# Performance work log

Measured on AMD Instinct MI355X. Metric: run time of the kernel, lower is better.

Reference implementation:

```python
import jax, jax.numpy as jnp
import numpy as np

B, S, HID, NH, HD = 2, 2048, 1024, 16, 64  # batch, seq, hidden, heads, head_dim (1024//NH)
ROPE_THETA = 10000.0
EPS = 1e-5


def _ternary_quantize(w):
    # BitNet b1.58 absmean weight quantization: ternary values + scalar scale.
    s = jnp.mean(jnp.abs(w)) + EPS
    q = jnp.clip(jnp.round(w / s), -1.0, 1.0)
    return q, s


def _rotate_half(x):
    x1, x2 = jnp.split(x, 2, axis=-1)
    return jnp.concatenate((-x2, x1), axis=-1)


def _rope_cos_sin(position_ids, head_dim, dtype):
    inv_freq = 1.0 / (ROPE_THETA ** (jnp.arange(0, head_dim, 2, dtype=jnp.float32) / head_dim))
    freqs = position_ids.astype(jnp.float32)[..., None] * inv_freq  # [b, s, hd/2]
    emb = jnp.concatenate((freqs, freqs), axis=-1)  # [b, s, hd]
    # add head axis -> [b, 1, s, hd]
    return jnp.cos(emb)[:, None].astype(dtype), jnp.sin(emb)[:, None].astype(dtype)


def setup_inputs() -> dict:
    key = jax.random.key(0)
    ks = jax.random.split(key, 5)
    hidden_states = jax.random.normal(ks[0], (B, S, HID), jnp.float32)
    hidden_states_scale = jnp.ones((1,), jnp.float32)
    position_ids = jnp.broadcast_to(jnp.arange(S, dtype=jnp.int32), (B, S))
    wq = jax.random.normal(ks[1], (HID, HID), jnp.float32) * 0.02
    wk = jax.random.normal(ks[2], (HID, HID), jnp.float32) * 0.02
    wv = jax.random.normal(ks[3], (HID, HID), jnp.float32) * 0.02
    wo = jax.random.normal(ks[4], (HID, HID), jnp.float32) * 0.02
    return {"hidden_states": hidden_states, "hidden_states_scale": hidden_states_scale,
            "position_ids": position_ids, "wq": wq, "wk": wk, "wv": wv, "wo": wo}


def reference(hidden_states, hidden_states_scale, position_ids, wq, wk, wv, wo):
    b, s, _ = hidden_states.shape
    hs_scale = hidden_states_scale.reshape(())

    # QuantizedLinear: ternary weight values, scale carried separately.
    wq_q, sq = _ternary_quantize(wq)
    wk_q, sk = _ternary_quantize(wk)
    wv_q, sv = _ternary_quantize(wv)
    wo_q, so = _ternary_quantize(wo)

    # Projections in the quantized-value domain: out = x @ Wq^T, out_scale = x_scale * w_scale
    q = jnp.einsum('bsh,oh->bso', hidden_states, wq_q)
    k = jnp.einsum('bsh,oh->bso', hidden_states, wk_q)
    v = jnp.einsum('bsh,oh->bso', hidden_states, wv_q)
    q_scale = hs_scale * sq
    k_scale = hs_scale * sk
    v_scale = hs_scale * sv

    # [b, nh, s, hd]
    q = q.reshape(b, s, NH, HD).transpose(0, 2, 1, 3)
    k = k.reshape(b, s, NH, HD).transpose(0, 2, 1, 3)
    v = v.reshape(b, s, NH, HD).transpose(0, 2, 1, 3)

    cos, sin = _rope_cos_sin(position_ids, HD, q.dtype)
    q = q * cos + _rotate_half(q) * sin
    k = k * cos + _rotate_half(k) * sin

    # quantized_matmul(Q, qs, K, ks): values multiply, scales multiply (scale unused by softmax,
    # matching the original which softmaxes the quantized-domain scores).
    attn = jnp.einsum('bhqd,bhkd->bhqk', q, k).astype(jnp.float32) * (1.0 / np.sqrt(HD))
    attn = jax.nn.softmax(attn, axis=-1)

    # quantized_matmul(attn, 1.0, V, vs)
    out = jnp.einsum('bhqk,bhkd->bhqd', attn, v.astype(jnp.float32))
    out_scale = 1.0 * v_scale

    out = out.transpose(0, 2, 1, 3).reshape(b, s, HID)
    out = jnp.einsum('bsh,oh->bso', out, wo_q)
    out_scale = out_scale * so
    return out, out_scale
```

## Files before the change

kernel.cpp:

```cpp
#include <hip/hip_runtime.h>
#include <hip/hip_bf16.h>

#define NB 2
#define NS 2048
#define NHID 1024
#define NHEAD 16
#define NHD 64
#define NTOK (NB*NS)
#define WELEM (NHID*NHID)

typedef unsigned short u16;
typedef __attribute__((ext_vector_type(4))) float floatx4;
typedef __attribute__((ext_vector_type(16))) float floatx16;
typedef __attribute__((ext_vector_type(8))) __bf16 bf16x8;
typedef __attribute__((ext_vector_type(8))) unsigned short ushort8;
typedef __attribute__((ext_vector_type(4))) unsigned short ushort4v;
typedef __attribute__((ext_vector_type(2))) unsigned uint2v;

__device__ __forceinline__ u16 f2bf(float f) {
  union { float f; unsigned u; } a; a.f = f;
  unsigned u = a.u;
  unsigned r = (u + 0x7fffu + ((u >> 16) & 1u)) >> 16;
  return (u16)r;
}
__device__ __forceinline__ float bf2f(u16 s) {
  union { unsigned u; float f; } a; a.u = ((unsigned)s) << 16;
  return a.f;
}
__device__ __forceinline__ void gload16(const void* g, void* lds) {
  __builtin_amdgcn_global_load_lds(
      (const __attribute__((address_space(1))) unsigned int*)g,
      (__attribute__((address_space(3))) unsigned int*)lds, 16, 0, 0);
}
__device__ __forceinline__ uint2v pl32(unsigned a, unsigned b) {
  return __builtin_amdgcn_permlane32_swap(a, b, false, false);
}
__device__ __forceinline__ float mergemax(float x) {
  uint2v r = pl32(__float_as_uint(x), __float_as_uint(x));
  return fmaxf(__uint_as_float(r[0]), __uint_as_float(r[1]));
}
__device__ __forceinline__ float mergesum(float x) {
  uint2v r = pl32(__float_as_uint(x), __float_as_uint(x));
  return __uint_as_float(r[0]) + __uint_as_float(r[1]);
}
__device__ __forceinline__ float tmax16(const floatx16& v) {
  float a = fmaxf(fmaxf(fmaxf(v[0], v[1]), fmaxf(v[2], v[3])),
                  fmaxf(fmaxf(v[4], v[5]), fmaxf(v[6], v[7])));
  float b = fmaxf(fmaxf(fmaxf(v[8], v[9]), fmaxf(v[10], v[11])),
                  fmaxf(fmaxf(v[12], v[13]), fmaxf(v[14], v[15])));
  return fmaxf(a, b);
}

__global__ void k_init(double* sums) { if (threadIdx.x < 4) sums[threadIdx.x] = 0.0; }

__global__ void k_abssum(const float* __restrict__ wq, const float* __restrict__ wk,
                         const float* __restrict__ wv, const float* __restrict__ wo,
                         double* __restrict__ sums) {
  const float* srcs[4] = {wq, wk, wv, wo};
  const float* w = srcs[blockIdx.y];
  int idx = (blockIdx.x * 256 + threadIdx.x) * 16;
  float s = 0.f;
#pragma unroll
  for (int j = 0; j < 4; j++) {
    float4 v = *(const float4*)(w + idx + j * 4);
    s += fabsf(v.x) + fabsf(v.y) + fabsf(v.z) + fabsf(v.w);
  }
#pragma unroll
  for (int off = 32; off; off >>= 1) s += __shfl_down(s, off);
  __shared__ float ps[4];
  if ((threadIdx.x & 63) == 0) ps[threadIdx.x >> 6] = s;
  __syncthreads();
  if (threadIdx.x == 0) atomicAdd(&sums[blockIdx.y], (double)(ps[0] + ps[1] + ps[2] + ps[3]));
}

__global__ void k_quantsplit(const float* __restrict__ wq, const float* __restrict__ wk,
                             const float* __restrict__ wv, const float* __restrict__ wo,
                             const double* __restrict__ sums, u16* __restrict__ wt,
                             const float* __restrict__ x,
                             u16* __restrict__ xh, u16* __restrict__ xl,
                             float2* __restrict__ rtab) {
  int bid = blockIdx.x;
  if (bid < 4096) {
    const float* srcs[4] = {wq, wk, wv, wo};
    int y = bid >> 10, xb = bid & 1023;
    const float* w = srcs[y];
    u16* dst = wt + y * WELEM;
    float s = (float)(sums[y] / (double)WELEM) + 1e-5f;
    int idx = (xb * 256 + threadIdx.x) * 4;
    float4 v = *(const float4*)(w + idx);
    float f[4] = {v.x, v.y, v.z, v.w};
    union { u16 ss[4]; uint2 u; } O;
#pragma unroll
    for (int j = 0; j < 4; j++) {
      float q = rintf(f[j] / s);
      q = fminf(1.f, fmaxf(-1.f, q));
      O.ss[j] = f2bf(q);
    }
    *(uint2*)(dst + idx) = O.u;
  } else if (bid < 8192) {
    int idx = ((bid - 4096) * 256 + threadIdx.x) * 4;
    float4 v = *(const float4*)(x + idx);
    float f[4] = {v.x, v.y, v.z, v.w};
    union { u16 s[4]; uint2 u; } H, L;
#pragma unroll
    for (int j = 0; j < 4; j++) {
      u16 hb = f2bf(f[j]);
      H.s[j] = hb;
      L.s[j] = f2bf(f[j] - bf2f(hb));
    }
    *(uint2*)(xh + idx) = H.u;
    *(uint2*)(xl + idx) = L.u;
  } else {
    int idx = (bid - 8192) * 256 + threadIdx.x;
    int d = idx & 31;
    float p = (float)(idx >> 5);
    float inv = exp2f((float)d * -0.4152410118609203f);
    float fr = p * inv;
    rtab[idx] = make_float2(cosf(fr), sinf(fr));
  }
}

template <int MODE>
__global__ __launch_bounds__(256) void k_gemm(
    const u16* __restrict__ Ahi, const u16* __restrict__ Alo,
    const u16* __restrict__ Wt, const int* __restrict__ pos_ids,
    const float2* __restrict__ rtab, float* __restrict__ outf,
    u16* __restrict__ qh, u16* __restrict__ ql,
    u16* __restrict__ kh, u16* __restrict__ kl,
    u16* __restrict__ vt) {
  constexpr int BUF = (MODE == 0) ? 24576 : 16384;
  __shared__ __attribute__((aligned(16))) char GSM[2 * BUF];
  const int tid = threadIdx.x;
  const int wave = tid >> 6, lane = tid & 63;
  const int lr = lane & 15, lh = lane >> 4;
  const int bm = blockIdx.x, bn = blockIdx.y, z = blockIdx.z;
  const u16* W = Wt + (MODE == 0 ? z : 3) * WELEM;
  const int wr = wave >> 1, wc = wave & 1;

  floatx4 acc[4][4];
#pragma unroll
  for (int i = 0; i < 4; i++)
#pragma unroll
    for (int j = 0; j < 4; j++) acc[i][j] = (floatx4){0.f, 0.f, 0.f, 0.f};

  const int e0 = tid * 8;
  const int row0 = e0 >> 5, col0 = e0 & 31;

  auto stage = [&](int k0, int nb) {
#pragma unroll
    for (int it = 0; it < 2; ++it) {
      int row = row0 + it * 64;
      gload16(Ahi + (bm * 128 + row) * 1024 + k0 + col0, GSM + nb + it * 4096 + wave * 1024);
      if (MODE == 0)
        gload16(Alo + (bm * 128 + row) * 1024 + k0 + col0, GSM + nb + 8192 + it * 4096 + wave * 1024);
      gload16(W + (bn * 128 + row) * 1024 + k0 + col0,
              GSM + nb + (MODE == 0 ? 16384 : 8192) + it * 4096 + wave * 1024);
    }
  };

  stage(0, 0);

  for (int kt = 0; kt < 32; ++kt) {
    __syncthreads();
    const int cb = (kt & 1) * BUF;
    if (kt < 31) stage((kt + 1) * 32, ((kt + 1) & 1) * BUF);

    const u16* Ahp = (const u16*)(GSM + cb);
    const u16* Bp  = (const u16*)(GSM + cb + (MODE == 0 ? 16384 : 8192));
    bf16x8 ah[4], bfr[4];
#pragma unroll
    for (int mi = 0; mi < 4; mi++)
      ah[mi] = *(const bf16x8*)(Ahp + (wr * 64 + mi * 16 + lr) * 32 + lh * 8);
#pragma unroll
    for (int ni = 0; ni < 4; ni++)
      bfr[ni] = *(const bf16x8*)(Bp + (wc * 64 + ni * 16 + lr) * 32 + lh * 8);
#pragma unroll
    for (int mi = 0; mi < 4; mi++)
#pragma unroll
      for (int ni = 0; ni < 4; ni++)
        acc[mi][ni] = __builtin_amdgcn_mfma_f32_16x16x32_bf16(ah[mi], bfr[ni], acc[mi][ni], 0, 0, 0);
    if (MODE == 0) {
      const u16* Alp = (const u16*)(GSM + cb + 8192);
      bf16x8 al8[4];
#pragma unroll
      for (int mi = 0; mi < 4; mi++)
        al8[mi] = *(const bf16x8*)(Alp + (wr * 64 + mi * 16 + lr) * 32 + lh * 8);
#pragma unroll
      for (int mi = 0; mi < 4; mi++)
#pragma unroll
        for (int ni = 0; ni < 4; ni++)
          acc[mi][ni] = __builtin_amdgcn_mfma_f32_16x16x32_bf16(al8[mi], bfr[ni], acc[mi][ni], 0, 0, 0);
    }
  }

  if (MODE == 1) {
#pragma unroll
    for (int mi = 0; mi < 4; mi++)
#pragma unroll
      for (int ni = 0; ni < 4; ni++)
#pragma unroll
        for (int i = 0; i < 4; i++) {
          int row = bm * 128 + wr * 64 + mi * 16 + lh * 4 + i;
          int col = bn * 128 + wc * 64 + ni * 16 + lr;
          outf[row * 1024 + col] = acc[mi][ni][i];
        }
    return;
  }

  const int hh = bn * 2 + wc;
  if (z == 2) {
#pragma unroll
    for (int mi = 0; mi < 4; mi++) {
      int row0v = bm * 128 + wr * 64 + mi * 16 + lh * 4;
      int bb = row0v >> 11, s_ = row0v & 2047;
      size_t vbase = ((size_t)(bb * NHEAD + hh)) * (NHD * NS) + s_;
#pragma unroll
      for (int ni = 0; ni < 4; ni++) {
        int hd = ni * 16 + lr;
        union { u16 s4[4]; ushort4v v; } V4;
#pragma unroll
        for (int i = 0; i < 4; i++) V4.s4[i] = f2bf(acc[mi][ni][i]);
        *(ushort4v*)(vt + vbase + (size_t)hd * NS) = V4.v;
      }
    }
    return;
  }

  const float qsc = (z == 0) ? 0.125f * 1.4426950408889634f : 1.0f;
  u16* dh = z ? kh : qh;
  u16* dl = z ? kl : ql;
  int posr[4][4];
#pragma unroll
  for (int mi = 0; mi < 4; mi++)
#pragma unroll
    for (int i = 0; i < 4; i++) {
      int row = bm * 128 + wr * 64 + mi * 16 + lh * 4 + i;
      posr[mi][i] = pos_ids[(row >> 11) * NS + (row & 2047)];
    }
#pragma unroll
  for (int ni = 0; ni < 2; ni++) {
    int d = ni * 16 + lr;
#pragma unroll
    for (int mi = 0; mi < 4; mi++)
#pragma unroll
      for (int i = 0; i < 4; i++) {
        int row = bm * 128 + wr * 64 + mi * 16 + lh * 4 + i;
        int bb = row >> 11, s_ = row & 2047;
        float2 cs = rtab[posr[mi][i] * 32 + d];
        float x1 = acc[mi][ni][i], x2 = acc[mi][ni + 2][i];
        float n1 = (x1 * cs.x - x2 * cs.y) * qsc;
        float n2 = (x2 * cs.x + x1 * cs.y) * qsc;
        size_t ob = ((size_t)(bb * NHEAD + hh) * NS + s_) * NHD + d;
        u16 h1 = f2bf(n1);
        dh[ob] = h1;      dl[ob] = f2bf(n1 - bf2f(h1));
        u16 h2 = f2bf(n2);
        dh[ob + 32] = h2; dl[ob + 32] = f2bf(n2 - bf2f(h2));
      }
  }
}

__global__ __launch_bounds__(512) void k_attn(
    const u16* __restrict__ qh, const u16* __restrict__ ql,
    const u16* __restrict__ kh, const u16* __restrict__ kl,
    const u16* __restrict__ vt, u16* __restrict__ aoh) {
  __shared__ __attribute__((aligned(16))) char SM[49152];
  const int tid = threadIdx.x, wave = tid >> 6, lane = tid & 63;
  const int l5 = lane & 31, hi = lane >> 5;
  const int bid = blockIdx.x;
  const int swzb = ((bid & 7) << 5) | (bid >> 3);
  const int qt = swzb & 7, bh = swzb >> 3;
  const int b = bh >> 4, hco = (bh & 15) * NHD;
  const int base = bh * (NS * NHD);
  const int qrow = qt * 256 + wave * 32 + l5;

  bf16x8 qfh[4], qfl[4];
#pragma unroll
  for (int s = 0; s < 4; s++) {
    int off = base + qrow * NHD + s * 16 + hi * 8;
    qfh[s] = *(const bf16x8*)(qh + off);
    qfl[s] = *(const bf16x8*)(ql + off);
  }

  const floatx16 Z16 = {};
  floatx16 acco[2];
  acco[0] = Z16; acco[1] = Z16;
  float m_r = -1e30f, l_r = 0.f;

  const char* khg0 = (const char*)(kh + base);
  const char* klg0 = (const char*)(kl + base);
  const char* vtg0 = (const char*)(vt + base);

#define STAGE_KV(key0_, nb_)                                                     \
  {                                                                              \
    const char* khg = khg0 + (key0_) * 128;                                      \
    const char* klg = klg0 + (key0_) * 128;                                      \
    const char* vtg = vtg0 + (key0_) * 2;                                        \
    int L = tid * 16;                                                            \
    int r7 = (L >> 7) & 7;                                                       \
    int g = L ^ (r7 << 4);                                                       \
    gload16(khg + g, SM + (nb_) + wave * 1024);                                  \
    gload16(klg + g, SM + (nb_) + 8192 + wave * 1024);                           \
    int vcol = (L & 127) ^ (r7 << 4);                                            \
    gload16(vtg + (size_t)(L >> 7) * 4096 + vcol,                                \
            SM + (nb_) + 16384 + wave * 1024);                                   \
  }

  STAGE_KV(0, 0);

  for (int kt = 0; kt < 32; ++kt) {
    __syncthreads();
    const int cb = (kt & 1) * 24576;
    const int key0 = kt * 64;

    if (kt < 31) STAGE_KV(key0 + 64, ((kt + 1) & 1) * 24576);

    floatx16 sacc[2];
#pragma unroll
    for (int t = 0; t < 2; t++) {
      const int row = 32 * t + l5;
      const int swz = (row & 7) << 4;
      {
        int byt = cb + row * 128 + ((hi * 16) ^ swz);
        bf16x8 ah = *(const bf16x8*)(SM + byt);
        bf16x8 al8 = *(const bf16x8*)(SM + 8192 + byt);
        __builtin_amdgcn_s_setprio(1);
        sacc[t] = __builtin_amdgcn_mfma_f32_32x32x16_bf16(ah, qfh[0], Z16, 0, 0, 0);
        sacc[t] = __builtin_amdgcn_mfma_f32_32x32x16_bf16(ah, qfl[0], sacc[t], 0, 0, 0);
        sacc[t] = __builtin_amdgcn_mfma_f32_32x32x16_bf16(al8, qfh[0], sacc[t], 0, 0, 0);
        __builtin_amdgcn_s_setprio(0);
      }
#pragma unroll
      for (int s = 1; s < 4; s++) {
        int byt = cb + row * 128 + ((s * 32 + hi * 16) ^ swz);
        bf16x8 ah = *(const bf16x8*)(SM + byt);
        bf16x8 al8 = *(const bf16x8*)(SM + 8192 + byt);
        __builtin_amdgcn_s_setprio(1);
        sacc[t] = __builtin_amdgcn_mfma_f32_32x32x16_bf16(ah, qfh[s], sacc[t], 0, 0, 0);
        sacc[t] = __builtin_amdgcn_mfma_f32_32x32x16_bf16(ah, qfl[s], sacc[t], 0, 0, 0);
        sacc[t] = __builtin_amdgcn_mfma_f32_32x32x16_bf16(al8, qfh[s], sacc[t], 0, 0, 0);
        __builtin_amdgcn_s_setprio(0);
      }
    }

    float mt = fmaxf(tmax16(sacc[0]), tmax16(sacc[1]));
    mt = mergemax(mt);
    if (!__all(mt <= m_r + 8.0f)) {
      float mn = fmaxf(m_r, mt);
      float sc2 = exp2f(m_r - mn);
      l_r *= sc2;
#pragma unroll
      for (int dt = 0; dt < 2; dt++)
#pragma unroll
        for (int r = 0; r < 16; r++) acco[dt][r] *= sc2;
      m_r = mn;
    }
    float s0 = 0.f, s1 = 0.f, s2 = 0.f, s3 = 0.f;
#pragma unroll
    for (int t = 0; t < 2; t++)
#pragma unroll
      for (int r = 0; r < 16; r += 4) {
        float p0 = exp2f(sacc[t][r + 0] - m_r);
        float p1 = exp2f(sacc[t][r + 1] - m_r);
        float p2 = exp2f(sacc[t][r + 2] - m_r);
        float p3 = exp2f(sacc[t][r + 3] - m_r);
        sacc[t][r + 0] = p0; sacc[t][r + 1] = p1;
        sacc[t][r + 2] = p2; sacc[t][r + 3] = p3;
        s0 += p0; s1 += p1; s2 += p2; s3 += p3;
      }
    l_r += mergesum((s0 + s1) + (s2 + s3));

    bf16x8 vtf[2][4];
#pragma unroll
    for (int dt = 0; dt < 2; dt++) {
      const int vrow = l5 + 32 * dt;
      const int swzv = (vrow & 7) << 4;
#pragma unroll
      for (int s = 0; s < 4; s++)
        vtf[dt][s] = *(const bf16x8*)(SM + cb + 16384 + vrow * 128 + ((s * 32 + hi * 16) ^ swzv));
    }

#pragma unroll
    for (int s = 0; s < 4; s++) {
      int t = s >> 1, rb = (s & 1) * 8;
      union { __bf16 bb[8]; unsigned u[4]; } Wp;
#pragma unroll
      for (int j = 0; j < 8; j++) Wp.bb[j] = (__bf16)sacc[t][rb + j];
      uint2v r02 = pl32(Wp.u[0], Wp.u[2]);
      uint2v r13 = pl32(Wp.u[1], Wp.u[3]);
      union { unsigned u[4]; bf16x8 v; } P;
      P.u[0] = r02[0]; P.u[1] = r13[0]; P.u[2] = r02[1]; P.u[3] = r13[1];
      __builtin_amdgcn_s_setprio(1);
      acco[0] = __builtin_amdgcn_mfma_f32_32x32x16_bf16(vtf[0][s], P.v, acco[0], 0, 0, 0);
      acco[1] = __builtin_amdgcn_mfma_f32_32x32x16_bf16(vtf[1][s], P.v, acco[1], 0, 0, 0);
      __builtin_amdgcn_s_setprio(0);
    }
  }

  float inv = 1.0f / l_r;
  float* OT = (float*)SM;
#pragma unroll
  for (int rnd = 0; rnd < 2; rnd++) {
    __syncthreads();
    if ((wave >> 2) == rnd) {
      int orow = (wave & 3) * 32 + l5;
#pragma unroll
      for (int dt = 0; dt < 2; dt++)
#pragma unroll
        for (int r = 0; r < 16; r++) {
          int col = (r & 3) + 8 * (r >> 2) + 4 * hi + 32 * dt;
          int cs = (col & 32) | ((col ^ l5) & 31);
          OT[orow * 64 + cs] = acco[dt][r] * inv;
        }
    }
    __syncthreads();
    {
      int row = tid >> 2, q4 = tid & 3;
      union { u16 s8[8]; ushort8 v; } HB[2];
#pragma unroll
      for (int j = 0; j < 16; j++) {
        int c = q4 * 16 + j;
        int cs = (c & 32) | ((c ^ (row & 31)) & 31);
        HB[j >> 3].s8[j & 7] = f2bf(OT[row * 64 + cs]);
      }
      int rowg = qt * 256 + rnd * 128 + row;
      size_t doff = ((size_t)(b * NS + rowg)) * NHID + hco + q4 * 16;
      *(ushort8*)(aoh + doff) = HB[0].v;
      *(ushort8*)(aoh + doff + 8) = HB[1].v;
    }
  }
}

__global__ void k_scale(const double* __restrict__ sums, const float* __restrict__ hss,
                        float* __restrict__ out) {
  if (threadIdx.x == 0) {
    float sv = (float)(sums[2] / (double)WELEM) + 1e-5f;
    float so = (float)(sums[3] / (double)WELEM) + 1e-5f;
    out[NTOK * NHID] = hss[0] * sv * so;
  }
}

extern "C" void kernel_launch(void* const* d_in, const int* in_sizes, int n_in,
                              void* d_out, int out_size, void* d_ws, size_t ws_size,
                              hipStream_t stream) {
  const float* x   = (const float*)d_in[0];
  const float* hss = (const float*)d_in[1];
  const int*   pos = (const int*)d_in[2];
  const float* wq  = (const float*)d_in[3];
  const float* wk  = (const float*)d_in[4];
  const float* wv  = (const float*)d_in[5];
  const float* wo  = (const float*)d_in[6];
  float* out = (float*)d_out;
  char* ws = (char*)d_ws;
  const size_t MB = 1u << 20;
  u16* wt = (u16*)(ws);
  u16* xh = (u16*)(ws + 8 * MB);
  u16* xl = (u16*)(ws + 16 * MB);
  u16* qh = (u16*)(ws + 24 * MB);
  u16* ql = (u16*)(ws + 32 * MB);
  u16* kh = (u16*)(ws + 40 * MB);
  u16* kl = (u16*)(ws + 48 * MB);
  u16* vt = (u16*)(ws + 56 * MB);
  double* sums = (double*)(ws + 72 * MB);
  float2* rtab = (float2*)(ws + 73 * MB);
  u16* aoh = xh;

  k_init<<<1, 64, 0, stream>>>(sums);
  k_abssum<<<dim3(256, 4), 256, 0, stream>>>(wq, wk, wv, wo, sums);
  k_quantsplit<<<8448, 256, 0, stream>>>(wq, wk, wv, wo, sums, wt, x, xh, xl, rtab);
  k_gemm<0><<<dim3(32, 8, 3), 256, 0, stream>>>(xh, xl, wt, pos, rtab, nullptr,
                                                qh, ql, kh, kl, vt);
  k_attn<<<256, 512, 0, stream>>>(qh, ql, kh, kl, vt, aoh);
  k_gemm<1><<<dim3(32, 8, 1), 256, 0, stream>>>(aoh, nullptr, wt, nullptr, nullptr, out,
                                                nullptr, nullptr, nullptr, nullptr, nullptr);
  k_scale<<<1, 64, 0, stream>>>(sums, hss, out);
}
```

Measured before the change: 204.1 us.

## Widen attention key tiles to 128, drop V low-part GEMM, fold scale kernel

The attention kernel now stages 128 keys per iteration instead of 64, doubling shared memory to 96KB and halving loop iterations and barriers. V fragments are read from LDS inside the PV loop rather than preloaded. The V projection skips its low-precision split MFMA pass, which halves its MMA work at some cost in accuracy. The init kernel becomes a memset and the scale kernel is folded into the output GEMM, removing launches. The larger LDS footprint may limit occupancy.

```diff
diff --git a/kernel.cpp b/kernel.cpp
--- a/kernel.cpp
+++ b/kernel.cpp
@@ -50,8 +50,6 @@
                   fmaxf(fmaxf(v[12], v[13]), fmaxf(v[14], v[15])));
   return fmaxf(a, b);
 }
-
-__global__ void k_init(double* sums) { if (threadIdx.x < 4) sums[threadIdx.x] = 0.0; }
 
 __global__ void k_abssum(const float* __restrict__ wq, const float* __restrict__ wk,
                          const float* __restrict__ wv, const float* __restrict__ wo,
@@ -127,7 +125,8 @@
     const float2* __restrict__ rtab, float* __restrict__ outf,
     u16* __restrict__ qh, u16* __restrict__ ql,
     u16* __restrict__ kh, u16* __restrict__ kl,
-    u16* __restrict__ vt) {
+    u16* __restrict__ vt,
+    const double* __restrict__ sums, const float* __restrict__ hss) {
   constexpr int BUF = (MODE == 0) ? 24576 : 16384;
   __shared__ __attribute__((aligned(16))) char GSM[2 * BUF];
   const int tid = threadIdx.x;
@@ -179,7 +178,7 @@
 #pragma unroll
       for (int ni = 0; ni < 4; ni++)
         acc[mi][ni] = __builtin_amdgcn_mfma_f32_16x16x32_bf16(ah[mi], bfr[ni], acc[mi][ni], 0, 0, 0);
-    if (MODE == 0) {
+    if (MODE == 0 && z != 2) {
       const u16* Alp = (const u16*)(GSM + cb + 8192);
       bf16x8 al8[4];
 #pragma unroll
@@ -204,6 +203,11 @@
           int col = bn * 128 + wc * 64 + ni * 16 + lr;
           outf[row * 1024 + col] = acc[mi][ni][i];
         }
+    if (bm == 0 && bn == 0 && tid == 0) {
+      float sv = (float)(sums[2] / (double)WELEM) + 1e-5f;
+      float so = (float)(sums[3] / (double)WELEM) + 1e-5f;
+      outf[NTOK * NHID] = hss[0] * sv * so;
+    }
     return;
   }
 
@@ -263,7 +267,7 @@
     const u16* __restrict__ qh, const u16* __restrict__ ql,
     const u16* __restrict__ kh, const u16* __restrict__ kl,
     const u16* __restrict__ vt, u16* __restrict__ aoh) {
-  __shared__ __attribute__((aligned(16))) char SM[49152];
+  __shared__ __attribute__((aligned(16))) char SM[98304];
   const int tid = threadIdx.x, wave = tid >> 6, lane = tid & 63;
   const int l5 = lane & 31, hi = lane >> 5;
   const int bid = blockIdx.x;
@@ -295,34 +299,37 @@
     const char* khg = khg0 + (key0_) * 128;                                      \
     const char* klg = klg0 + (key0_) * 128;                                      \
     const char* vtg = vtg0 + (key0_) * 2;                                        \
-    int L = tid * 16;                                                            \
-    int r7 = (L >> 7) & 7;                                                       \
-    int g = L ^ (r7 << 4);                                                       \
-    gload16(khg + g, SM + (nb_) + wave * 1024);                                  \
-    gload16(klg + g, SM + (nb_) + 8192 + wave * 1024);                           \
-    int vcol = (L & 127) ^ (r7 << 4);                                            \
-    gload16(vtg + (size_t)(L >> 7) * 4096 + vcol,                                \
-            SM + (nb_) + 16384 + wave * 1024);                                   \
+    _Pragma("unroll")                                                            \
+    for (int it = 0; it < 2; ++it) {                                             \
+      int L = it * 8192 + tid * 16;                                              \
+      int r7 = (L >> 7) & 7;                                                     \
+      int g = L ^ (r7 << 4);                                                     \
+      int dst = (nb_) + it * 8192 + wave * 1024;                                 \
+      gload16(khg + g, SM + dst);                                                \
+      gload16(klg + g, SM + 16384 + dst);                                        \
+      int vcol = (L & 255) ^ (((L >> 8) & 15) << 4);                             \
+      gload16(vtg + (size_t)(L >> 8) * 4096 + vcol, SM + 32768 + dst);           \
+    }                                                                            \
   }
 
   STAGE_KV(0, 0);
 
-  for (int kt = 0; kt < 32; ++kt) {
+  for (int kt = 0; kt < 16; ++kt) {
     __syncthreads();
-    const int cb = (kt & 1) * 24576;
-    const int key0 = kt * 64;
-
-    if (kt < 31) STAGE_KV(key0 + 64, ((kt + 1) & 1) * 24576);
-
-    floatx16 sacc[2];
-#pragma unroll
-    for (int t = 0; t < 2; t++) {
+    const int cb = (kt & 1) * 49152;
+    const int key0 = kt * 128;
+
+    if (kt < 15) STAGE_KV(key0 + 128, ((kt + 1) & 1) * 49152);
+
+    floatx16 sacc[4];
+#pragma unroll
+    for (int t = 0; t < 4; t++) {
       const int row = 32 * t + l5;
       const int swz = (row & 7) << 4;
       {
         int byt = cb + row * 128 + ((hi * 16) ^ swz);
         bf16x8 ah = *(const bf16x8*)(SM + byt);
-        bf16x8 al8 = *(const bf16x8*)(SM + 8192 + byt);
+        bf16x8 al8 = *(const bf16x8*)(SM + 16384 + byt);
         __builtin_amdgcn_s_setprio(1);
         sacc[t] = __builtin_amdgcn_mfma_f32_32x32x16_bf16(ah, qfh[0], Z16, 0, 0, 0);
         sacc[t] = __builtin_amdgcn_mfma_f32_32x32x16_bf16(ah, qfl[0], sacc[t], 0, 0, 0);
@@ -333,7 +340,7 @@
       for (int s = 1; s < 4; s++) {
         int byt = cb + row * 128 + ((s * 32 + hi * 16) ^ swz);
         bf16x8 ah = *(const bf16x8*)(SM + byt);
-        bf16x8 al8 = *(const bf16x8*)(SM + 8192 + byt);
+        bf16x8 al8 = *(const bf16x8*)(SM + 16384 + byt);
         __builtin_amdgcn_s_setprio(1);
         sacc[t] = __builtin_amdgcn_mfma_f32_32x32x16_bf16(ah, qfh[s], sacc[t], 0, 0, 0);
         sacc[t] = __builtin_amdgcn_mfma_f32_32x32x16_bf16(ah, qfl[s], sacc[t], 0, 0, 0);
@@ -342,7 +349,8 @@
       }
     }
 
-    float mt = fmaxf(tmax16(sacc[0]), tmax16(sacc[1]));
+    float mt = fmaxf(fmaxf(tmax16(sacc[0]), tmax16(sacc[1])),
+                     fmaxf(tmax16(sacc[2]), tmax16(sacc[3])));
     mt = mergemax(mt);
     if (!__all(mt <= m_r + 8.0f)) {
       float mn = fmaxf(m_r, mt);
@@ -356,7 +364,7 @@
     }
     float s0 = 0.f, s1 = 0.f, s2 = 0.f, s3 = 0.f;
 #pragma unroll
-    for (int t = 0; t < 2; t++)
+    for (int t = 0; t < 4; t++)
 #pragma unroll
       for (int r = 0; r < 16; r += 4) {
         float p0 = exp2f(sacc[t][r + 0] - m_r);
@@ -369,18 +377,8 @@
       }
     l_r += mergesum((s0 + s1) + (s2 + s3));
 
-    bf16x8 vtf[2][4];
-#pragma unroll
-    for (int dt = 0; dt < 2; dt++) {
-      const int vrow = l5 + 32 * dt;
-      const int swzv = (vrow & 7) << 4;
-#pragma unroll
-      for (int s = 0; s < 4; s++)
-        vtf[dt][s] = *(const bf16x8*)(SM + cb + 16384 + vrow * 128 + ((s * 32 + hi * 16) ^ swzv));
-    }
-
-#pragma unroll
-    for (int s = 0; s < 4; s++) {
+#pragma unroll
+    for (int s = 0; s < 8; s++) {
       int t = s >> 1, rb = (s & 1) * 8;
       union { __bf16 bb[8]; unsigned u[4]; } Wp;
 #pragma unroll
@@ -389,9 +387,12 @@
       uint2v r13 = pl32(Wp.u[1], Wp.u[3]);
       union { unsigned u[4]; bf16x8 v; } P;
       P.u[0] = r02[0]; P.u[1] = r13[0]; P.u[2] = r02[1]; P.u[3] = r13[1];
+      const int coloff = (s * 32 + hi * 16) ^ ((l5 & 15) << 4);
+      bf16x8 v0 = *(const bf16x8*)(SM + cb + 32768 + l5 * 256 + coloff);
+      bf16x8 v1 = *(const bf16x8*)(SM + cb + 32768 + (l5 + 32) * 256 + coloff);
       __builtin_amdgcn_s_setprio(1);
-      acco[0] = __builtin_amdgcn_mfma_f32_32x32x16_bf16(vtf[0][s], P.v, acco[0], 0, 0, 0);
-      acco[1] = __builtin_amdgcn_mfma_f32_32x32x16_bf16(vtf[1][s], P.v, acco[1], 0, 0, 0);
+      acco[0] = __builtin_amdgcn_mfma_f32_32x32x16_bf16(v0, P.v, acco[0], 0, 0, 0);
+      acco[1] = __builtin_amdgcn_mfma_f32_32x32x16_bf16(v1, P.v, acco[1], 0, 0, 0);
       __builtin_amdgcn_s_setprio(0);
     }
   }
@@ -427,15 +428,6 @@
       *(ushort8*)(aoh + doff) = HB[0].v;
       *(ushort8*)(aoh + doff + 8) = HB[1].v;
     }
-  }
-}
-
-__global__ void k_scale(const double* __restrict__ sums, const float* __restrict__ hss,
-                        float* __restrict__ out) {
-  if (threadIdx.x == 0) {
-    float sv = (float)(sums[2] / (double)WELEM) + 1e-5f;
-    float so = (float)(sums[3] / (double)WELEM) + 1e-5f;
-    out[NTOK * NHID] = hss[0] * sv * so;
   }
 }
 
@@ -464,13 +456,13 @@
   float2* rtab = (float2*)(ws + 73 * MB);
   u16* aoh = xh;
 
-  k_init<<<1, 64, 0, stream>>>(sums);
+  hipMemsetAsync(sums, 0, 4 * sizeof(double), stream);
   k_abssum<<<dim3(256, 4), 256, 0, stream>>>(wq, wk, wv, wo, sums);
   k_quantsplit<<<8448, 256, 0, stream>>>(wq, wk, wv, wo, sums, wt, x, xh, xl, rtab);
   k_gemm<0><<<dim3(32, 8, 3), 256, 0, stream>>>(xh, xl, wt, pos, rtab, nullptr,
-                                                qh, ql, kh, kl, vt);
+                                                qh, ql, kh, kl, vt, nullptr, nullptr);
   k_attn<<<256, 512, 0, stream>>>(qh, ql, kh, kl, vt, aoh);
   k_gemm<1><<<dim3(32, 8, 1), 256, 0, stream>>>(aoh, nullptr, wt, nullptr, nullptr, out,
-                                                nullptr, nullptr, nullptr, nullptr, nullptr);
-  k_scale<<<1, 64, 0, stream>>>(sums, hss, out);
-}
+                                                nullptr, nullptr, nullptr, nullptr, nullptr,
+                                                sums, hss);
+}
```

New measurement: 198.9 us. 2.6% less time.
